# Kernel optimization log

Measured on AMD Instinct MI355X. Metric: run time of the kernel, lower is better.

## Reference

```python
import jax, jax.numpy as jnp
import numpy as np

B = 4            # batch size
W_BEV = 512      # bev_width
H_BEV = 512      # bev_height
M = 200000       # total pillars (divisible by B)
N = 2000000      # total points
C_IN = 10        # mlps[0]
C_OUT = 64       # mlps[-1]
BN_EPS = 1e-3


def setup_inputs() -> dict:
    key = jax.random.key(0)
    ks = jax.random.split(key, 6)
    group_features = jax.random.normal(ks[0], (N, C_IN), dtype=jnp.float32)
    # every pillar gets at least one point; remaining points land randomly
    extra = jax.random.randint(ks[1], (N - M,), 0, M, dtype=jnp.int32)
    pillar_set_indices = jnp.concatenate([jnp.arange(M, dtype=jnp.int32), extra])
    # unique (batch, x, y) coords per pillar: per-batch unique linear slots
    Mb = M // B
    lin = jnp.concatenate([
        jax.random.permutation(jax.random.fold_in(ks[2], b), W_BEV * H_BEV)[:Mb]
        for b in range(B)
    ])  # (M,)
    batch_ids = jnp.repeat(jnp.arange(B), Mb)
    pillar_indices = jnp.stack([batch_ids, lin // H_BEV, lin % H_BEV], axis=1).astype(jnp.int32)
    # params (xavier-ish scaling)
    W0 = jax.random.normal(ks[3], (C_IN, C_OUT), dtype=jnp.float32) * np.sqrt(2.0 / (C_IN + C_OUT))
    gamma = jnp.ones((C_OUT,), dtype=jnp.float32)
    beta = jnp.zeros((C_OUT,), dtype=jnp.float32)
    Ws = jax.random.normal(ks[4], (C_OUT, C_OUT), dtype=jnp.float32) * np.sqrt(2.0 / (2 * C_OUT))
    bs = jnp.zeros((C_OUT,), dtype=jnp.float32)
    return {
        "group_features": group_features,
        "pillar_set_indices": pillar_set_indices,
        "pillar_indices": pillar_indices,
        "W0": W0, "gamma": gamma, "beta": beta, "Ws": Ws, "bs": bs,
    }


def reference(group_features, pillar_set_indices, pillar_indices, W0, gamma, beta, Ws, bs):
    idx = pillar_set_indices.astype(jnp.int32)
    # shared MLP: Linear(bias=False) -> BatchNorm1d(train-mode batch stats) -> ReLU
    h = group_features @ W0                                   # (N, C_OUT)
    mu = jnp.mean(h, axis=0)
    var = jnp.var(h, axis=0)                                  # biased, as BN training
    h = jax.nn.relu((h - mu) * jax.lax.rsqrt(var + BN_EPS) * gamma + beta)
    # attentive score
    s = jax.nn.relu(h @ Ws + bs)                              # (N, C_OUT)
    # scatter_softmax over points within each pillar, per channel
    smax = jax.ops.segment_max(s, idx, num_segments=M)        # (M, C_OUT)
    e = jnp.exp(s - smax[idx])
    denom = jax.ops.segment_sum(e, idx, num_segments=M)
    attn = e / denom[idx]
    # scatter_sum of attention-weighted features + scatter_max
    p1 = jax.ops.segment_sum(h * attn, idx, num_segments=M)   # (M, C_OUT)
    p2 = jax.ops.segment_max(h, idx, num_segments=M)          # (M, C_OUT)
    pillar_features = 0.5 * (p1 + p2)
    # dense BEV canvas scatter: indices = b*(W*H) + x*H + y (unique by construction)
    flat = (pillar_indices[:, 0].astype(jnp.int32) * (W_BEV * H_BEV)
            + pillar_indices[:, 1].astype(jnp.int32) * H_BEV
            + pillar_indices[:, 2].astype(jnp.int32))
    canvas = jnp.zeros((B * W_BEV * H_BEV, C_OUT), dtype=pillar_features.dtype)
    canvas = canvas.at[flat].set(pillar_features)
    return canvas.reshape(B, W_BEV, H_BEV, C_OUT).transpose(0, 3, 1, 2)  # (B, C, W, H)
```

## Files before the change

### kernel.cpp

```cpp
#include <hip/hip_runtime.h>
#include <stdint.h>

#define C_INP 10
#define CH    64
#define WBEV  512
#define HBEV  512
#define BQ    4
#define WH    (WBEV*HBEV)
#define BN_EPS 1e-3f
#define WIN   224
#define SCHUNK 1024

typedef unsigned short ushort8 __attribute__((ext_vector_type(8)));
typedef short  bf16x8 __attribute__((ext_vector_type(8)));
typedef float  f32x4  __attribute__((ext_vector_type(4)));

__device__ __forceinline__ unsigned short f2b(float x) {
  unsigned int u = __float_as_uint(x);
  return (unsigned short)((u + 0x7FFFu + ((u >> 16) & 1u)) >> 16);
}
__device__ __forceinline__ float b2f(unsigned short u) {
  return __uint_as_float(((unsigned int)u) << 16);
}

__global__ __launch_bounds__(256, 1)
void k_stats(const float* __restrict__ X, int N, float* __restrict__ sums) {
  float a[65];
#pragma unroll
  for (int i = 0; i < 65; ++i) a[i] = 0.f;
  const int stride = gridDim.x * blockDim.x;
  for (int i = blockIdx.x * blockDim.x + threadIdx.x; i < N; i += stride) {
    const float* xr = X + (size_t)i * C_INP;
    float x[C_INP];
#pragma unroll
    for (int k = 0; k < C_INP; ++k) x[k] = xr[k];
#pragma unroll
    for (int k = 0; k < C_INP; ++k) a[k] += x[k];
#pragma unroll
    for (int k = 0; k < C_INP; ++k)
#pragma unroll
      for (int l = k; l < C_INP; ++l)
        a[C_INP + (k * (21 - k)) / 2 + (l - k)] = fmaf(x[k], x[l], a[C_INP + (k * (21 - k)) / 2 + (l - k)]);
  }
  __shared__ float red[4 * 65];
  const int wv = threadIdx.x >> 6;
#pragma unroll
  for (int i = 0; i < 65; ++i) {
    float v = a[i];
    v += __shfl_down(v, 32, 64);
    v += __shfl_down(v, 16, 64);
    v += __shfl_down(v, 8, 64);
    v += __shfl_down(v, 4, 64);
    v += __shfl_down(v, 2, 64);
    v += __shfl_down(v, 1, 64);
    if ((threadIdx.x & 63) == 0) red[wv * 65 + i] = v;
  }
  __syncthreads();
  const int t = threadIdx.x;
  if (t < 65) atomicAdd(&sums[t], red[t] + red[65 + t] + red[130 + t] + red[195 + t]);
}

__global__ void k_bnfold(const float* __restrict__ sums, const float* __restrict__ W0,
                         const float* __restrict__ gamma, const float* __restrict__ beta,
                         float Nf, float* __restrict__ W0p, float* __restrict__ b0p) {
  const int c = threadIdx.x;
  float w[C_INP];
#pragma unroll
  for (int k = 0; k < C_INP; ++k) w[k] = W0[k * CH + c];
  float mu = 0.f;
#pragma unroll
  for (int k = 0; k < C_INP; ++k) mu += (sums[k] / Nf) * w[k];
  float ex2 = 0.f;
  int ti = C_INP;
#pragma unroll
  for (int k = 0; k < C_INP; ++k)
#pragma unroll
    for (int l = k; l < C_INP; ++l) {
      const float s = sums[ti++] / Nf;
      ex2 += (k == l ? w[k] * w[k] : 2.f * w[k] * w[l]) * s;
    }
  const float var = ex2 - mu * mu;
  const float sc = gamma[c] * rsqrtf(var + BN_EPS);
#pragma unroll
  for (int k = 0; k < C_INP; ++k) W0p[k * CH + c] = w[k] * sc;
  b0p[c] = beta[c] - mu * sc;
}

__global__ void k_count(const int* __restrict__ idx, int N, int* __restrict__ counts) {
  const int i = blockIdx.x * 256 + threadIdx.x;
  if (i < N) atomicAdd(&counts[idx[i]], 1);
}

__global__ __launch_bounds__(256)
void k_scan1(const int* __restrict__ counts, int M, int* __restrict__ bsum) {
  __shared__ int lds[256];
  const int b = blockIdx.x, t = threadIdx.x;
  const int base = b * SCHUNK + t * 4;
  int s = 0;
  if (base + 3 < M) {
    const int4 v = *(const int4*)(counts + base);
    s = v.x + v.y + v.z + v.w;
  } else {
#pragma unroll
    for (int j = 0; j < 4; ++j) if (base + j < M) s += counts[base + j];
  }
  lds[t] = s;
  __syncthreads();
  for (int o = 1; o < 256; o <<= 1) {
    const int u = (t >= o) ? lds[t - o] : 0;
    __syncthreads();
    lds[t] += u;
    __syncthreads();
  }
  if (t == 255) bsum[b] = lds[255];
}

__global__ __launch_bounds__(256)
void k_scan2(int* __restrict__ bsum, int nsb) {
  __shared__ int lds[256];
  const int t = threadIdx.x;
  const int v = (t < nsb) ? bsum[t] : 0;
  lds[t] = v;
  __syncthreads();
  for (int o = 1; o < 256; o <<= 1) {
    const int u = (t >= o) ? lds[t - o] : 0;
    __syncthreads();
    lds[t] += u;
    __syncthreads();
  }
  if (t < nsb) bsum[t] = lds[t] - v;
}

__global__ __launch_bounds__(256)
void k_scan3(const int* __restrict__ counts, int M, int N,
             const int* __restrict__ bsum,
             int* __restrict__ off, int* __restrict__ head) {
  __shared__ int lds[256];
  const int b = blockIdx.x, t = threadIdx.x;
  const int base = b * SCHUNK + t * 4;
  int c0 = 0, c1 = 0, c2 = 0, c3 = 0;
  const bool full = (base + 3 < M);
  if (full) {
    const int4 v = *(const int4*)(counts + base);
    c0 = v.x; c1 = v.y; c2 = v.z; c3 = v.w;
  } else {
    if (base     < M) c0 = counts[base];
    if (base + 1 < M) c1 = counts[base + 1];
    if (base + 2 < M) c2 = counts[base + 2];
    if (base + 3 < M) c3 = counts[base + 3];
  }
  const int s = c0 + c1 + c2 + c3;
  lds[t] = s;
  __syncthreads();
  for (int o = 1; o < 256; o <<= 1) {
    const int u = (t >= o) ? lds[t - o] : 0;
    __syncthreads();
    lds[t] += u;
    __syncthreads();
  }
  const int run = bsum[b] + lds[t] - s;
  const int4 ov = {run, run + c0, run + c0 + c1, run + c0 + c1 + c2};
  if (full) {
    *(int4*)(off  + base) = ov;
    *(int4*)(head + base) = ov;
  } else {
    if (base     < M) { off[base]     = ov.x; head[base]     = ov.x; }
    if (base + 1 < M) { off[base + 1] = ov.y; head[base + 1] = ov.y; }
    if (base + 2 < M) { off[base + 2] = ov.z; head[base + 2] = ov.z; }
  }
  if (b == 0 && t == 0) off[M] = N;
}

__global__ void k_fill(const int* __restrict__ idx, int N, int* __restrict__ head,
                       int* __restrict__ plist) {
  const int i = blockIdx.x * 256 + threadIdx.x;
  if (i < N) {
    const int p = idx[i];
    const int pos = atomicAdd(&head[p], 1);
    plist[pos] = i;
  }
}

__global__ __launch_bounds__(64)
void k_zb(const int* __restrict__ idx, const int* __restrict__ plist, int N,
          float* __restrict__ num, float* __restrict__ den, float* __restrict__ hmx) {
  const int b = blockIdx.x;
  const int c = threadIdx.x;
  const int w0 = b * WIN;
  const int w1 = min(w0 + WIN, N);
  const int p0 = idx[plist[w0]];
  const int p1 = idx[plist[w1 - 1]];
  const size_t o0 = (size_t)p0 * CH + c;
  const size_t o1 = (size_t)p1 * CH + c;
  num[o0] = 0.f; den[o0] = 0.f; hmx[o0] = 0.f;
  num[o1] = 0.f; den[o1] = 0.f; hmx[o1] = 0.f;
}

__global__ void k_invmap(const int* __restrict__ pind, int M, int* __restrict__ inv) {
  const int p = blockIdx.x * 256 + threadIdx.x;
  if (p < M) {
    const int b = pind[3 * p], x = pind[3 * p + 1], y = pind[3 * p + 2];
    inv[(size_t)b * WH + x * HBEV + y] = p;
  }
}

__global__ __launch_bounds__(256, 2)
void k_main(const float* __restrict__ X,
            const int* __restrict__ plist, const int* __restrict__ idx,
            const int* __restrict__ off,
            const float* __restrict__ W0p, const float* __restrict__ b0p,
            const float* __restrict__ Ws, const float* __restrict__ bs,
            float* __restrict__ num, float* __restrict__ den, float* __restrict__ hmx,
            int N, int M) {
  __shared__ __attribute__((aligned(16))) unsigned short sm[2 * WIN * 72];
  unsigned short* hB = sm;
  unsigned short* eB = sm + WIN * 72;
  const int t = threadIdx.x;
  const int w0 = blockIdx.x * WIN;
  const int w1 = min(w0 + WIN, N);

  if (t < WIN && w0 + t < N) {
    const int pid = plist[w0 + t];
    const float* xr = X + (size_t)pid * C_INP;
    float x[C_INP];
#pragma unroll
    for (int k = 0; k < C_INP; ++k) x[k] = xr[k];
    float h[CH];
#pragma unroll
    for (int c = 0; c < CH; ++c) {
      float a = b0p[c];
#pragma unroll
      for (int k = 0; k < C_INP; ++k) a = fmaf(x[k], W0p[k * CH + c], a);
      h[c] = fmaxf(a, 0.f);
    }
    ushort8* dst = (ushort8*)(hB + t * 72);
#pragma unroll
    for (int i = 0; i < 8; ++i) {
      ushort8 v;
#pragma unroll
      for (int j = 0; j < 8; ++j) v[j] = f2b(h[i * 8 + j]);
      dst[i] = v;
    }
  }

  const int wv = t >> 6, lane = t & 63;
  const int l15 = lane & 15, quad = (lane >> 4) & 3;
  const int nCol = wv * 16 + l15;
  bf16x8 bf0, bf1;
#pragma unroll
  for (int j = 0; j < 8; ++j) {
    bf0[j] = (short)f2b(Ws[(quad * 8 + j) * CH + nCol]);
    bf1[j] = (short)f2b(Ws[(32 + quad * 8 + j) * CH + nCol]);
  }
  const float bsv = bs[nCol];
  __syncthreads();

#pragma unroll 2
  for (int mt = 0; mt < WIN / 16; ++mt) {
    const bf16x8 a0 = *(const bf16x8*)(hB + (mt * 16 + l15) * 72 + quad * 8);
    const bf16x8 a1 = *(const bf16x8*)(hB + (mt * 16 + l15) * 72 + 32 + quad * 8);
    f32x4 acc = {0.f, 0.f, 0.f, 0.f};
    acc = __builtin_amdgcn_mfma_f32_16x16x32_bf16(a0, bf0, acc, 0, 0, 0);
    acc = __builtin_amdgcn_mfma_f32_16x16x32_bf16(a1, bf1, acc, 0, 0, 0);
#pragma unroll
    for (int r = 0; r < 4; ++r) {
      const float e = __expf(fmaxf(acc[r] + bsv, 0.f));
      eB[(mt * 16 + quad * 4 + r) * 72 + nCol] = f2b(e);
    }
  }
  __syncthreads();

  const int c = lane;
  const int pfirst = idx[plist[w0]];
  const int plast  = idx[plist[w1 - 1]];
  for (int p = pfirst + wv; p <= plast; p += 4) {
    const int pb = off[p], pe = off[p + 1];
    const int l2 = max(pb, w0) - w0;
    const int h2 = min(pe, w1) - w0;
    if (h2 <= l2) continue;
    float dn = 0.f, nm = 0.f, hm = 0.f;
    for (int r = l2; r < h2; ++r) {
      const float hv = b2f(hB[r * 72 + c]);
      const float ev = b2f(eB[r * 72 + c]);
      dn += ev;
      nm = fmaf(hv, ev, nm);
      hm = fmaxf(hm, hv);
    }
    const size_t o = (size_t)p * CH + c;
    if (pb >= w0 && pe <= w1) {
      num[o] = nm; den[o] = dn; hmx[o] = hm;
    } else {
      atomicAdd(num + o, nm);
      atomicAdd(den + o, dn);
      atomicMax((int*)hmx + o, __float_as_int(hm));
    }
  }
}

__global__ __launch_bounds__(256)
void k_canvas(const int* __restrict__ inv, const float* __restrict__ num,
              const float* __restrict__ den, const float* __restrict__ hmx,
              float* __restrict__ out) {
  const int t = threadIdx.x;
  const int bid = blockIdx.x;
  const int half = bid & 1;
  const int x = (bid >> 1) & (WBEV - 1);
  const int b = bid >> 10;
  const int ybase = half * 256;
  const size_t cell = (size_t)b * WH + (size_t)x * HBEV + ybase + t;
  const int iv = inv[cell];
  const size_t obase = (size_t)b * ((size_t)CH * WH) + (size_t)x * HBEV + ybase + t;
  if (iv >= 0) {
    const float4* np = (const float4*)(num + (size_t)iv * CH);
    const float4* dp = (const float4*)(den + (size_t)iv * CH);
    const float4* mp = (const float4*)(hmx + (size_t)iv * CH);
#pragma unroll 4
    for (int cq = 0; cq < 16; ++cq) {
      const float4 n = np[cq], d = dp[cq], m = mp[cq];
      out[obase + (size_t)(4 * cq + 0) * WH] = 0.5f * (n.x / d.x + m.x);
      out[obase + (size_t)(4 * cq + 1) * WH] = 0.5f * (n.y / d.y + m.y);
      out[obase + (size_t)(4 * cq + 2) * WH] = 0.5f * (n.z / d.z + m.z);
      out[obase + (size_t)(4 * cq + 3) * WH] = 0.5f * (n.w / d.w + m.w);
    }
  } else {
#pragma unroll 8
    for (int cc = 0; cc < CH; ++cc) out[obase + (size_t)cc * WH] = 0.f;
  }
}

extern "C" void kernel_launch(void* const* d_in, const int* in_sizes, int n_in,
                              void* d_out, int out_size, void* d_ws, size_t ws_size,
                              hipStream_t stream) {
  const float* X     = (const float*)d_in[0];
  const int*   idx   = (const int*)  d_in[1];
  const int*   pind  = (const int*)  d_in[2];
  const float* W0    = (const float*)d_in[3];
  const float* gamma = (const float*)d_in[4];
  const float* beta  = (const float*)d_in[5];
  const float* Ws    = (const float*)d_in[6];
  const float* bs    = (const float*)d_in[7];
  float* out = (float*)d_out;
  const int N = in_sizes[0] / C_INP;
  const int M = in_sizes[2] / 3;
  const int nwin = (N + WIN - 1) / WIN;
  const int nsb  = (M + SCHUNK - 1) / SCHUNK;

  char* p = (char*)d_ws;
  auto carve = [&](size_t bytes) -> char* {
    char* r = p;
    p += (bytes + 255) & ~(size_t)255;
    return r;
  };
  int*   counts = (int*)  carve((size_t)M * 4);
  int*   off    = (int*)  carve((size_t)(M + 1) * 4);
  int*   head   = (int*)  carve((size_t)M * 4);
  int*   plist  = (int*)  carve((size_t)N * 4);
  int*   bsum   = (int*)  carve((size_t)256 * 4);
  float* sums   = (float*)carve(65 * 4);
  float* W0p    = (float*)carve((size_t)C_INP * CH * 4);
  float* b0p    = (float*)carve((size_t)CH * 4);
  float* num    = (float*)carve((size_t)M * CH * 4);
  float* den    = (float*)carve((size_t)M * CH * 4);
  float* hmx    = (float*)carve((size_t)M * CH * 4);
  int*   inv    = (int*)  carve((size_t)BQ * WH * 4);

  hipMemsetAsync(counts, 0, (size_t)M * 4, stream);
  hipMemsetAsync(sums, 0, 65 * 4, stream);
  hipMemsetAsync(inv, 0xFF, (size_t)BQ * WH * 4, stream);

  k_stats <<<1024, 256, 0, stream>>>(X, N, sums);
  k_bnfold<<<1, 64, 0, stream>>>(sums, W0, gamma, beta, (float)N, W0p, b0p);
  k_count <<<(N + 255) / 256, 256, 0, stream>>>(idx, N, counts);
  k_scan1 <<<nsb, 256, 0, stream>>>(counts, M, bsum);
  k_scan2 <<<1, 256, 0, stream>>>(bsum, nsb);
  k_scan3 <<<nsb, 256, 0, stream>>>(counts, M, N, bsum, off, head);
  k_fill  <<<(N + 255) / 256, 256, 0, stream>>>(idx, N, head, plist);
  k_zb    <<<nwin, 64, 0, stream>>>(idx, plist, N, num, den, hmx);
  k_invmap<<<(M + 255) / 256, 256, 0, stream>>>(pind, M, inv);
  k_main  <<<nwin, 256, 0, stream>>>(X, plist, idx, off, W0p, b0p,
                                     Ws, bs, num, den, hmx, N, M);
  k_canvas<<<BQ * WBEV * 2, 256, 0, stream>>>(inv, num, den, hmx, out);
}
```

Before: 967.4 us.

## Use MFMA for first layer, pack weights, interleave accumulators, fuse count into stats

The first linear layer plus BN fold now runs on bf16 MFMA, with the bias folded in as an extra input column. A new one-block kernel pre-packs the W0 and Ws fragments. Pillar counting moves into the stats kernel, and zeroing of boundary pillars moves into the scan kernel, removing the separate count and zero kernels. num/den/max are interleaved into a single 192-float row per pillar for better locality in the canvas gather. The window shrinks to 160 with three blocks per CU to raise occupancy; the bf16 inputs to the first layer reduce precision.

```diff
diff --git a/kernel.cpp b/kernel.cpp
--- a/kernel.cpp
+++ b/kernel.cpp
@@ -8,7 +8,8 @@
 #define BQ    4
 #define WH    (WBEV*HBEV)
 #define BN_EPS 1e-3f
-#define WIN   224
+#define WIN   160
+#define TILES (WIN/16)
 #define SCHUNK 1024
 
 typedef unsigned short ushort8 __attribute__((ext_vector_type(8)));
@@ -24,7 +25,8 @@
 }
 
 __global__ __launch_bounds__(256, 1)
-void k_stats(const float* __restrict__ X, int N, float* __restrict__ sums) {
+void k_stats(const float* __restrict__ X, const int* __restrict__ idx, int N,
+             float* __restrict__ sums, int* __restrict__ counts) {
   float a[65];
 #pragma unroll
   for (int i = 0; i < 65; ++i) a[i] = 0.f;
@@ -33,7 +35,11 @@
     const float* xr = X + (size_t)i * C_INP;
     float x[C_INP];
 #pragma unroll
-    for (int k = 0; k < C_INP; ++k) x[k] = xr[k];
+    for (int k = 0; k < C_INP; k += 2) {
+      const float2 v = *(const float2*)(xr + k);
+      x[k] = v.x; x[k + 1] = v.y;
+    }
+    atomicAdd(&counts[idx[i]], 1);
 #pragma unroll
     for (int k = 0; k < C_INP; ++k) a[k] += x[k];
 #pragma unroll
@@ -86,9 +92,27 @@
   b0p[c] = beta[c] - mu * sc;
 }
 
-__global__ void k_count(const int* __restrict__ idx, int N, int* __restrict__ counts) {
-  const int i = blockIdx.x * 256 + threadIdx.x;
-  if (i < N) atomicAdd(&counts[idx[i]], 1);
+__global__ __launch_bounds__(256)
+void k_pack(const float* __restrict__ W0p, const float* __restrict__ b0p,
+            const float* __restrict__ Ws,
+            unsigned short* __restrict__ w0f, unsigned short* __restrict__ wsf) {
+  const int t = threadIdx.x;
+  const int lane = t & 63, tile = t >> 6;
+  const int quad = lane >> 4, l15 = lane & 15;
+  const int col = tile * 16 + l15;
+#pragma unroll
+  for (int j = 0; j < 8; ++j) {
+    const int k = quad * 8 + j;
+    const float v = (k < C_INP) ? W0p[k * CH + col] : (k == C_INP ? b0p[col] : 0.f);
+    w0f[(tile * 64 + lane) * 8 + j] = f2b(v);
+  }
+#pragma unroll
+  for (int half = 0; half < 2; ++half)
+#pragma unroll
+    for (int j = 0; j < 8; ++j) {
+      const int k = half * 32 + quad * 8 + j;
+      wsf[((half * 4 + tile) * 64 + lane) * 8 + j] = f2b(Ws[k * CH + col]);
+    }
 }
 
 __global__ __launch_bounds__(256)
@@ -134,7 +158,8 @@
 __global__ __launch_bounds__(256)
 void k_scan3(const int* __restrict__ counts, int M, int N,
              const int* __restrict__ bsum,
-             int* __restrict__ off, int* __restrict__ head) {
+             int* __restrict__ off, int* __restrict__ head,
+             float* __restrict__ nda) {
   __shared__ int lds[256];
   const int b = blockIdx.x, t = threadIdx.x;
   const int base = b * SCHUNK + t * 4;
@@ -169,6 +194,17 @@
     if (base + 2 < M) { off[base + 2] = ov.z; head[base + 2] = ov.z; }
   }
   if (b == 0 && t == 0) off[M] = N;
+  const int st[4] = {ov.x, ov.y, ov.z, ov.w};
+  const int cn[4] = {c0, c1, c2, c3};
+#pragma unroll
+  for (int q = 0; q < 4; ++q) {
+    if (base + q < M && cn[q] > 0 && (st[q] / WIN) != ((st[q] + cn[q] - 1) / WIN)) {
+      float4* z = (float4*)(nda + (size_t)(base + q) * 192);
+      const float4 zz = {0.f, 0.f, 0.f, 0.f};
+#pragma unroll
+      for (int j = 0; j < 48; ++j) z[j] = zz;
+    }
+  }
 }
 
 __global__ void k_fill(const int* __restrict__ idx, int N, int* __restrict__ head,
@@ -181,21 +217,6 @@
   }
 }
 
-__global__ __launch_bounds__(64)
-void k_zb(const int* __restrict__ idx, const int* __restrict__ plist, int N,
-          float* __restrict__ num, float* __restrict__ den, float* __restrict__ hmx) {
-  const int b = blockIdx.x;
-  const int c = threadIdx.x;
-  const int w0 = b * WIN;
-  const int w1 = min(w0 + WIN, N);
-  const int p0 = idx[plist[w0]];
-  const int p1 = idx[plist[w1 - 1]];
-  const size_t o0 = (size_t)p0 * CH + c;
-  const size_t o1 = (size_t)p1 * CH + c;
-  num[o0] = 0.f; den[o0] = 0.f; hmx[o0] = 0.f;
-  num[o1] = 0.f; den[o1] = 0.f; hmx[o1] = 0.f;
-}
-
 __global__ void k_invmap(const int* __restrict__ pind, int M, int* __restrict__ inv) {
   const int p = blockIdx.x * 256 + threadIdx.x;
   if (p < M) {
@@ -204,64 +225,75 @@
   }
 }
 
-__global__ __launch_bounds__(256, 2)
+__global__ __launch_bounds__(256, 3)
 void k_main(const float* __restrict__ X,
             const int* __restrict__ plist, const int* __restrict__ idx,
             const int* __restrict__ off,
-            const float* __restrict__ W0p, const float* __restrict__ b0p,
-            const float* __restrict__ Ws, const float* __restrict__ bs,
-            float* __restrict__ num, float* __restrict__ den, float* __restrict__ hmx,
-            int N, int M) {
+            const unsigned short* __restrict__ w0f,
+            const unsigned short* __restrict__ wsf,
+            const float* __restrict__ bs,
+            float* __restrict__ nda, int N, int M) {
   __shared__ __attribute__((aligned(16))) unsigned short sm[2 * WIN * 72];
   unsigned short* hB = sm;
   unsigned short* eB = sm + WIN * 72;
   const int t = threadIdx.x;
   const int w0 = blockIdx.x * WIN;
   const int w1 = min(w0 + WIN, N);
-
-  if (t < WIN && w0 + t < N) {
-    const int pid = plist[w0 + t];
-    const float* xr = X + (size_t)pid * C_INP;
-    float x[C_INP];
-#pragma unroll
-    for (int k = 0; k < C_INP; ++k) x[k] = xr[k];
-    float h[CH];
-#pragma unroll
-    for (int c = 0; c < CH; ++c) {
-      float a = b0p[c];
-#pragma unroll
-      for (int k = 0; k < C_INP; ++k) a = fmaf(x[k], W0p[k * CH + c], a);
-      h[c] = fmaxf(a, 0.f);
-    }
-    ushort8* dst = (ushort8*)(hB + t * 72);
-#pragma unroll
-    for (int i = 0; i < 8; ++i) {
-      ushort8 v;
-#pragma unroll
-      for (int j = 0; j < 8; ++j) v[j] = f2b(h[i * 8 + j]);
-      dst[i] = v;
-    }
-  }
-
   const int wv = t >> 6, lane = t & 63;
   const int l15 = lane & 15, quad = (lane >> 4) & 3;
+
+  const bf16x8 w0b0 = *(const bf16x8*)(w0f + (0 * 64 + lane) * 8);
+  const bf16x8 w0b1 = *(const bf16x8*)(w0f + (1 * 64 + lane) * 8);
+  const bf16x8 w0b2 = *(const bf16x8*)(w0f + (2 * 64 + lane) * 8);
+  const bf16x8 w0b3 = *(const bf16x8*)(w0f + (3 * 64 + lane) * 8);
+  for (int mt = wv; mt < TILES; mt += 4) {
+    const int row = mt * 16 + l15;
+    const int gi = min(w0 + row, N - 1);
+    const int pid = plist[gi];
+    const float* xr = X + (size_t)pid * C_INP;
+    bf16x8 af = {0, 0, 0, 0, 0, 0, 0, 0};
+    if (quad == 0) {
+      const float2 p0 = *(const float2*)(xr);
+      const float2 p1 = *(const float2*)(xr + 2);
+      const float2 p2 = *(const float2*)(xr + 4);
+      const float2 p3 = *(const float2*)(xr + 6);
+      af[0] = (short)f2b(p0.x); af[1] = (short)f2b(p0.y);
+      af[2] = (short)f2b(p1.x); af[3] = (short)f2b(p1.y);
+      af[4] = (short)f2b(p2.x); af[5] = (short)f2b(p2.y);
+      af[6] = (short)f2b(p3.x); af[7] = (short)f2b(p3.y);
+    } else if (quad == 1) {
+      const float2 p4 = *(const float2*)(xr + 8);
+      af[0] = (short)f2b(p4.x); af[1] = (short)f2b(p4.y);
+      af[2] = (short)0x3F80;
+    }
+    f32x4 a0 = {0.f, 0.f, 0.f, 0.f}, a1 = a0, a2 = a0, a3 = a0;
+    a0 = __builtin_amdgcn_mfma_f32_16x16x32_bf16(af, w0b0, a0, 0, 0, 0);
+    a1 = __builtin_amdgcn_mfma_f32_16x16x32_bf16(af, w0b1, a1, 0, 0, 0);
+    a2 = __builtin_amdgcn_mfma_f32_16x16x32_bf16(af, w0b2, a2, 0, 0, 0);
+    a3 = __builtin_amdgcn_mfma_f32_16x16x32_bf16(af, w0b3, a3, 0, 0, 0);
+#pragma unroll
+    for (int r = 0; r < 4; ++r) {
+      unsigned short* hr = hB + (mt * 16 + quad * 4 + r) * 72 + l15;
+      hr[0]  = f2b(fmaxf(a0[r], 0.f));
+      hr[16] = f2b(fmaxf(a1[r], 0.f));
+      hr[32] = f2b(fmaxf(a2[r], 0.f));
+      hr[48] = f2b(fmaxf(a3[r], 0.f));
+    }
+  }
+
+  const bf16x8 bf0 = *(const bf16x8*)(wsf + ((0 * 4 + wv) * 64 + lane) * 8);
+  const bf16x8 bf1 = *(const bf16x8*)(wsf + ((1 * 4 + wv) * 64 + lane) * 8);
   const int nCol = wv * 16 + l15;
-  bf16x8 bf0, bf1;
-#pragma unroll
-  for (int j = 0; j < 8; ++j) {
-    bf0[j] = (short)f2b(Ws[(quad * 8 + j) * CH + nCol]);
-    bf1[j] = (short)f2b(Ws[(32 + quad * 8 + j) * CH + nCol]);
-  }
   const float bsv = bs[nCol];
   __syncthreads();
 
 #pragma unroll 2
-  for (int mt = 0; mt < WIN / 16; ++mt) {
-    const bf16x8 a0 = *(const bf16x8*)(hB + (mt * 16 + l15) * 72 + quad * 8);
-    const bf16x8 a1 = *(const bf16x8*)(hB + (mt * 16 + l15) * 72 + 32 + quad * 8);
+  for (int mt = 0; mt < TILES; ++mt) {
+    const bf16x8 A0 = *(const bf16x8*)(hB + (mt * 16 + l15) * 72 + quad * 8);
+    const bf16x8 A1 = *(const bf16x8*)(hB + (mt * 16 + l15) * 72 + 32 + quad * 8);
     f32x4 acc = {0.f, 0.f, 0.f, 0.f};
-    acc = __builtin_amdgcn_mfma_f32_16x16x32_bf16(a0, bf0, acc, 0, 0, 0);
-    acc = __builtin_amdgcn_mfma_f32_16x16x32_bf16(a1, bf1, acc, 0, 0, 0);
+    acc = __builtin_amdgcn_mfma_f32_16x16x32_bf16(A0, bf0, acc, 0, 0, 0);
+    acc = __builtin_amdgcn_mfma_f32_16x16x32_bf16(A1, bf1, acc, 0, 0, 0);
 #pragma unroll
     for (int r = 0; r < 4; ++r) {
       const float e = __expf(fmaxf(acc[r] + bsv, 0.f));
@@ -286,20 +318,19 @@
       nm = fmaf(hv, ev, nm);
       hm = fmaxf(hm, hv);
     }
-    const size_t o = (size_t)p * CH + c;
+    float* row = nda + (size_t)p * 192;
     if (pb >= w0 && pe <= w1) {
-      num[o] = nm; den[o] = dn; hmx[o] = hm;
+      row[c] = nm; row[64 + c] = dn; row[128 + c] = hm;
     } else {
-      atomicAdd(num + o, nm);
-      atomicAdd(den + o, dn);
-      atomicMax((int*)hmx + o, __float_as_int(hm));
+      atomicAdd(row + c, nm);
+      atomicAdd(row + 64 + c, dn);
+      atomicMax((int*)row + 128 + c, __float_as_int(hm));
     }
   }
 }
 
 __global__ __launch_bounds__(256)
-void k_canvas(const int* __restrict__ inv, const float* __restrict__ num,
-              const float* __restrict__ den, const float* __restrict__ hmx,
+void k_canvas(const int* __restrict__ inv, const float* __restrict__ nda,
               float* __restrict__ out) {
   const int t = threadIdx.x;
   const int bid = blockIdx.x;
@@ -311,9 +342,9 @@
   const int iv = inv[cell];
   const size_t obase = (size_t)b * ((size_t)CH * WH) + (size_t)x * HBEV + ybase + t;
   if (iv >= 0) {
-    const float4* np = (const float4*)(num + (size_t)iv * CH);
-    const float4* dp = (const float4*)(den + (size_t)iv * CH);
-    const float4* mp = (const float4*)(hmx + (size_t)iv * CH);
+    const float4* np = (const float4*)(nda + (size_t)iv * 192);
+    const float4* dp = np + 16;
+    const float4* mp = np + 32;
 #pragma unroll 4
     for (int cq = 0; cq < 16; ++cq) {
       const float4 n = np[cq], d = dp[cq], m = mp[cq];
@@ -359,25 +390,23 @@
   float* sums   = (float*)carve(65 * 4);
   float* W0p    = (float*)carve((size_t)C_INP * CH * 4);
   float* b0p    = (float*)carve((size_t)CH * 4);
-  float* num    = (float*)carve((size_t)M * CH * 4);
-  float* den    = (float*)carve((size_t)M * CH * 4);
-  float* hmx    = (float*)carve((size_t)M * CH * 4);
+  unsigned short* w0f = (unsigned short*)carve((size_t)4 * 64 * 8 * 2);
+  unsigned short* wsf = (unsigned short*)carve((size_t)8 * 64 * 8 * 2);
+  float* nda    = (float*)carve((size_t)M * 192 * 4);
   int*   inv    = (int*)  carve((size_t)BQ * WH * 4);
 
   hipMemsetAsync(counts, 0, (size_t)M * 4, stream);
   hipMemsetAsync(sums, 0, 65 * 4, stream);
   hipMemsetAsync(inv, 0xFF, (size_t)BQ * WH * 4, stream);
 
-  k_stats <<<1024, 256, 0, stream>>>(X, N, sums);
+  k_stats <<<1024, 256, 0, stream>>>(X, idx, N, sums, counts);
   k_bnfold<<<1, 64, 0, stream>>>(sums, W0, gamma, beta, (float)N, W0p, b0p);
-  k_count <<<(N + 255) / 256, 256, 0, stream>>>(idx, N, counts);
+  k_pack  <<<1, 256, 0, stream>>>(W0p, b0p, Ws, w0f, wsf);
   k_scan1 <<<nsb, 256, 0, stream>>>(counts, M, bsum);
   k_scan2 <<<1, 256, 0, stream>>>(bsum, nsb);
-  k_scan3 <<<nsb, 256, 0, stream>>>(counts, M, N, bsum, off, head);
+  k_scan3 <<<nsb, 256, 0, stream>>>(counts, M, N, bsum, off, head, nda);
   k_fill  <<<(N + 255) / 256, 256, 0, stream>>>(idx, N, head, plist);
-  k_zb    <<<nwin, 64, 0, stream>>>(idx, plist, N, num, den, hmx);
   k_invmap<<<(M + 255) / 256, 256, 0, stream>>>(pind, M, inv);
-  k_main  <<<nwin, 256, 0, stream>>>(X, plist, idx, off, W0p, b0p,
-                                     Ws, bs, num, den, hmx, N, M);
-  k_canvas<<<BQ * WBEV * 2, 256, 0, stream>>>(inv, num, den, hmx, out);
-}
+  k_main  <<<nwin, 256, 0, stream>>>(X, plist, idx, off, w0f, wsf, bs, nda, N, M);
+  k_canvas<<<BQ * WBEV * 2, 256, 0, stream>>>(inv, nda, out);
+}
```

New measurement: 930.2 us. -3.8%, faster.
